# Kernel optimization log

Hardware: AMD Instinct MI355X
Metric: run time of the kernel (lower is better)

Reference implementation:

```python
import jax, jax.numpy as jnp
import numpy as np

EMBED_DIM = 128
D3 = EMBED_DIM // 3  # 42
K = 3  # k = min(3, N-1); N >> 4 so k is statically 3


def _local_density(points):
    # points: [B, N, 3] -> mean distance to 3 nearest neighbors, [B, N, 1]
    sq = jnp.sum(points * points, axis=-1)  # [B, N]
    d2 = sq[:, :, None] + sq[:, None, :] - 2.0 * jnp.einsum('bnd,bmd->bnm', points, points)
    dists = jnp.sqrt(jnp.maximum(d2, 1e-12))  # [B, N, N]
    N = points.shape[1]
    eye = jnp.eye(N, dtype=bool)
    dists = jnp.where(eye[None, :, :], jnp.inf, dists)
    # k smallest = -(k largest of negated)
    neg_topk, _ = jax.lax.top_k(-dists, K)  # [B, N, K]
    return jnp.mean(-neg_topk, axis=-1, keepdims=True)  # [B, N, 1]


def setup_inputs() -> dict:
    key = jax.random.key(0)
    ks = jax.random.split(key, 9)
    B, N = 8, 4096
    points = jax.random.normal(ks[0], (B, N, 3), dtype=jnp.float32)
    # PyTorch Linear init scale: U(-1/sqrt(fan_in), 1/sqrt(fan_in))
    def lin(k, fan_in, fan_out):
        k1, k2 = jax.random.split(k)
        bnd = 1.0 / np.sqrt(fan_in)
        W = jax.random.uniform(k1, (fan_in, fan_out), jnp.float32, -bnd, bnd)
        b = jax.random.uniform(k2, (fan_out,), jnp.float32, -bnd, bnd)
        return W, b
    W_rel, b_rel = lin(ks[1], 3, D3)
    W_dist, b_dist = lin(ks[2], 1, D3)
    W_dens, b_dens = lin(ks[3], 1, D3)
    W_out, b_out = lin(ks[4], 3 * D3, EMBED_DIM)
    return {"points": points, "W_rel": W_rel, "b_rel": b_rel,
            "W_dist": W_dist, "b_dist": b_dist, "W_dens": W_dens, "b_dens": b_dens,
            "W_out": W_out, "b_out": b_out}


def reference(points, W_rel, b_rel, W_dist, b_dist, W_dens, b_dens, W_out, b_out):
    centroid = jnp.mean(points, axis=1, keepdims=True)          # [B, 1, 3]
    relative_pos = points - centroid                             # [B, N, 3]
    rel_features = relative_pos @ W_rel + b_rel                  # [B, N, D3]
    centroid_dist = jnp.linalg.norm(relative_pos, axis=-1, keepdims=True)  # [B, N, 1]
    dist_features = centroid_dist @ W_dist + b_dist              # [B, N, D3]
    local_density = _local_density(points)                       # [B, N, 1]
    density_features = local_density @ W_dens + b_dens           # [B, N, D3]
    features = jnp.concatenate([rel_features, dist_features, density_features], axis=-1)
    return features @ W_out + b_out                              # [B, N, 128]
```

## Files before the change

kernel.cpp:

```cpp
#include <hip/hip_runtime.h>
#include <math.h>

#define NPTS 4096
#define NBATCH 8

#define WS_CENT 0
#define WS_COEF 32

__global__ void prep_kernel(const float* __restrict__ pts,
                            const float* __restrict__ W_rel, const float* __restrict__ b_rel,
                            const float* __restrict__ W_dist, const float* __restrict__ b_dist,
                            const float* __restrict__ W_dens, const float* __restrict__ b_dens,
                            const float* __restrict__ W_out, const float* __restrict__ b_out,
                            float* __restrict__ ws) {
    __shared__ float sx[256], sy[256], sz[256];
    if (blockIdx.x < NBATCH) {
        int b = blockIdx.x;
        const float* P = pts + (size_t)b * NPTS * 3;
        float ax = 0.f, ay = 0.f, az = 0.f;
        for (int n = threadIdx.x; n < NPTS; n += 256) {
            ax += P[3 * n + 0];
            ay += P[3 * n + 1];
            az += P[3 * n + 2];
        }
        sx[threadIdx.x] = ax; sy[threadIdx.x] = ay; sz[threadIdx.x] = az;
        __syncthreads();
        for (int off = 128; off > 0; off >>= 1) {
            if (threadIdx.x < off) {
                sx[threadIdx.x] += sx[threadIdx.x + off];
                sy[threadIdx.x] += sy[threadIdx.x + off];
                sz[threadIdx.x] += sz[threadIdx.x + off];
            }
            __syncthreads();
        }
        if (threadIdx.x == 0) {
            const float inv = 1.0f / (float)NPTS;
            ws[WS_CENT + 4 * b + 0] = sx[0] * inv;
            ws[WS_CENT + 4 * b + 1] = sy[0] * inv;
            ws[WS_CENT + 4 * b + 2] = sz[0] * inv;
        }
    } else if (threadIdx.x < 128) {
        int o = threadIdx.x;
        float a0 = 0.f, a1 = 0.f, a2 = 0.f, vd = 0.f, vl = 0.f, be = b_out[o];
        for (int j = 0; j < 42; ++j) {
            float w0 = W_out[j * 128 + o];
            float w1 = W_out[(42 + j) * 128 + o];
            float w2 = W_out[(84 + j) * 128 + o];
            a0 = fmaf(W_rel[j],      w0, a0);
            a1 = fmaf(W_rel[42 + j], w0, a1);
            a2 = fmaf(W_rel[84 + j], w0, a2);
            vd = fmaf(W_dist[j],     w1, vd);
            vl = fmaf(W_dens[j],     w2, vl);
            be = fmaf(b_rel[j], w0, be);
            be = fmaf(b_dist[j], w1, be);
            be = fmaf(b_dens[j], w2, be);
        }
        float* C = ws + WS_COEF;
        C[0 * 128 + o] = a0;
        C[1 * 128 + o] = a1;
        C[2 * 128 + o] = a2;
        C[3 * 128 + o] = vd;
        C[4 * 128 + o] = vl;
        C[5 * 128 + o] = be;
    }
}

#define INS3(t0, t1, t2, v)                                   \
    {                                                         \
        float n0 = fminf(t0, (v));                            \
        float n1 = __builtin_amdgcn_fmed3f(t0, t1, (v));      \
        float n2 = __builtin_amdgcn_fmed3f(t1, t2, (v));      \
        t0 = n0; t1 = n1; t2 = n2;                            \
    }

#define MERGE3(t0, t1, t2, m)                                 \
    {                                                         \
        float b0 = __shfl_xor(t0, m);                         \
        float b1 = __shfl_xor(t1, m);                         \
        float b2 = __shfl_xor(t2, m);                         \
        float X = fmaxf(t0, b0);                              \
        t0 = fminf(t0, b0);                                   \
        float Y = fminf(t1, b1);                              \
        float Z = fmaxf(X, Y);                                \
        t1 = fminf(X, Y);                                     \
        t2 = fminf(Z, fminf(t2, b2));                         \
    }

__launch_bounds__(1024, 8)
__global__ void density_out_kernel(const float* __restrict__ pts,
                                   const float* __restrict__ ws,
                                   float* __restrict__ out) {
    __shared__ float4 lp4[NPTS];
    __shared__ float dens[64];
    int b = blockIdx.x >> 6;
    int g = blockIdx.x & 63;
    int tid = threadIdx.x;

    {
        const float4* P4 = (const float4*)(pts + (size_t)b * NPTS * 3);
        float4 v0 = P4[3 * tid + 0];
        float4 v1 = P4[3 * tid + 1];
        float4 v2 = P4[3 * tid + 2];
        float x0 = v0.x, y0 = v0.y, z0 = v0.z;
        float x1 = v0.w, y1 = v1.x, z1 = v1.y;
        float x2 = v1.z, y2 = v1.w, z2 = v2.x;
        float x3 = v2.y, y3 = v2.z, z3 = v2.w;
        lp4[4 * tid + 0] = make_float4(x0, y0, z0, fmaf(x0, x0, fmaf(y0, y0, z0 * z0)));
        lp4[4 * tid + 1] = make_float4(x1, y1, z1, fmaf(x1, x1, fmaf(y1, y1, z1 * z1)));
        lp4[4 * tid + 2] = make_float4(x2, y2, z2, fmaf(x2, x2, fmaf(y2, y2, z2 * z2)));
        lp4[4 * tid + 3] = make_float4(x3, y3, z3, fmaf(x3, x3, fmaf(y3, y3, z3 * z3)));
    }
    __syncthreads();

    int w = tid >> 6;
    int lane = tid & 63;
    int lw = w << 2;
    int qb = (g << 6) + lw;

    float4 Q0 = lp4[qb + 0];
    float4 Q1 = lp4[qb + 1];
    float4 Q2 = lp4[qb + 2];
    float4 Q3 = lp4[qb + 3];
    float q0x = -2.f * Q0.x, q0y = -2.f * Q0.y, q0z = -2.f * Q0.z;
    float q1x = -2.f * Q1.x, q1y = -2.f * Q1.y, q1z = -2.f * Q1.z;
    float q2x = -2.f * Q2.x, q2y = -2.f * Q2.y, q2z = -2.f * Q2.z;
    float q3x = -2.f * Q3.x, q3y = -2.f * Q3.y, q3z = -2.f * Q3.z;

    float t00 = INFINITY, t01 = INFINITY, t02 = INFINITY;
    float t10 = INFINITY, t11 = INFINITY, t12 = INFINITY;
    float t20 = INFINITY, t21 = INFINITY, t22 = INFINITY;
    float t30 = INFINITY, t31 = INFINITY, t32 = INFINITY;

    #pragma unroll 4
    for (int tile = 0; tile < 64; ++tile) {
        float4 c = lp4[(tile << 6) + lane];
        float e0 = fmaf(q0x, c.x, fmaf(q0y, c.y, fmaf(q0z, c.z, c.w)));
        float e1 = fmaf(q1x, c.x, fmaf(q1y, c.y, fmaf(q1z, c.z, c.w)));
        float e2 = fmaf(q2x, c.x, fmaf(q2y, c.y, fmaf(q2z, c.z, c.w)));
        float e3 = fmaf(q3x, c.x, fmaf(q3y, c.y, fmaf(q3z, c.z, c.w)));
        INS3(t00, t01, t02, e0);
        INS3(t10, t11, t12, e1);
        INS3(t20, t21, t22, e2);
        INS3(t30, t31, t32, e3);
    }

    if (lane == lw + 0) { t00 = t01; t01 = t02; t02 = INFINITY; }
    if (lane == lw + 1) { t10 = t11; t11 = t12; t12 = INFINITY; }
    if (lane == lw + 2) { t20 = t21; t21 = t22; t22 = INFINITY; }
    if (lane == lw + 3) { t30 = t31; t31 = t32; t32 = INFINITY; }

    #pragma unroll
    for (int m = 1; m < 64; m <<= 1) {
        MERGE3(t00, t01, t02, m);
        MERGE3(t10, t11, t12, m);
        MERGE3(t20, t21, t22, m);
        MERGE3(t30, t31, t32, m);
    }

    if (lane == 0) {
        dens[lw + 0] = (sqrtf(fmaxf(t00 + Q0.w, 1e-12f)) + sqrtf(fmaxf(t01 + Q0.w, 1e-12f)) +
                        sqrtf(fmaxf(t02 + Q0.w, 1e-12f))) * (1.0f / 3.0f);
        dens[lw + 1] = (sqrtf(fmaxf(t10 + Q1.w, 1e-12f)) + sqrtf(fmaxf(t11 + Q1.w, 1e-12f)) +
                        sqrtf(fmaxf(t12 + Q1.w, 1e-12f))) * (1.0f / 3.0f);
        dens[lw + 2] = (sqrtf(fmaxf(t20 + Q2.w, 1e-12f)) + sqrtf(fmaxf(t21 + Q2.w, 1e-12f)) +
                        sqrtf(fmaxf(t22 + Q2.w, 1e-12f))) * (1.0f / 3.0f);
        dens[lw + 3] = (sqrtf(fmaxf(t30 + Q3.w, 1e-12f)) + sqrtf(fmaxf(t31 + Q3.w, 1e-12f)) +
                        sqrtf(fmaxf(t32 + Q3.w, 1e-12f))) * (1.0f / 3.0f);
    }
    __syncthreads();

    int r = tid >> 4;
    int c8 = (tid & 15) << 3;
    float4 p = lp4[(g << 6) + r];
    float cx = ws[WS_CENT + 4 * b + 0];
    float cy = ws[WS_CENT + 4 * b + 1];
    float cz = ws[WS_CENT + 4 * b + 2];
    float rx = p.x - cx, ry = p.y - cy, rz = p.z - cz;
    float cd = sqrtf(fmaf(rx, rx, fmaf(ry, ry, rz * rz)));
    float ld = dens[r];
    const float* C = ws + WS_COEF;
    float* orow = out + ((size_t)(b * NPTS + (g << 6) + r)) * 128;
    #pragma unroll
    for (int h = 0; h < 2; ++h) {
        int o = c8 + 4 * h;
        float4 A0 = *(const float4*)(C + 0 * 128 + o);
        float4 A1 = *(const float4*)(C + 1 * 128 + o);
        float4 A2 = *(const float4*)(C + 2 * 128 + o);
        float4 VD = *(const float4*)(C + 3 * 128 + o);
        float4 VL = *(const float4*)(C + 4 * 128 + o);
        float4 BE = *(const float4*)(C + 5 * 128 + o);
        float4 rv;
        rv.x = fmaf(rx, A0.x, fmaf(ry, A1.x, fmaf(rz, A2.x, fmaf(cd, VD.x, fmaf(ld, VL.x, BE.x)))));
        rv.y = fmaf(rx, A0.y, fmaf(ry, A1.y, fmaf(rz, A2.y, fmaf(cd, VD.y, fmaf(ld, VL.y, BE.y)))));
        rv.z = fmaf(rx, A0.z, fmaf(ry, A1.z, fmaf(rz, A2.z, fmaf(cd, VD.z, fmaf(ld, VL.z, BE.z)))));
        rv.w = fmaf(rx, A0.w, fmaf(ry, A1.w, fmaf(rz, A2.w, fmaf(cd, VD.w, fmaf(ld, VL.w, BE.w)))));
        *(float4*)(orow + o) = rv;
    }
}

extern "C" void kernel_launch(void* const* d_in, const int* in_sizes, int n_in,
                              void* d_out, int out_size, void* d_ws, size_t ws_size,
                              hipStream_t stream) {
    const float* pts    = (const float*)d_in[0];
    const float* W_rel  = (const float*)d_in[1];
    const float* b_rel  = (const float*)d_in[2];
    const float* W_dist = (const float*)d_in[3];
    const float* b_dist = (const float*)d_in[4];
    const float* W_dens = (const float*)d_in[5];
    const float* b_dens = (const float*)d_in[6];
    const float* W_out  = (const float*)d_in[7];
    const float* b_out  = (const float*)d_in[8];
    float* out = (float*)d_out;
    float* ws  = (float*)d_ws;

    hipLaunchKernelGGL(prep_kernel, dim3(NBATCH + 1), dim3(256), 0, stream,
                       pts, W_rel, b_rel, W_dist, b_dist, W_dens, b_dens, W_out, b_out, ws);
    hipLaunchKernelGGL(density_out_kernel, dim3(NBATCH * 64), dim3(1024), 0, stream,
                       pts, ws, out);
}
```

Baseline: 38.95 us.

## Fuse prep into density kernel, compute centroid and coefficients per block, 8 queries per wave

Removes the separate prep kernel: each block now computes the batch centroid with wave shuffles and redundantly folds the weight matrices into LDS coefficients. Each wave now handles 8 query points instead of 4, using readfirstlane to keep query coordinates scalar, which halves the grid to 256 blocks of 1024 threads. This saves a kernel launch and the global workspace round trip, and reuses each candidate LDS load across more queries. The costs are redundant weight folding in every block, fewer blocks to fill the device, and higher register pressure.

```diff
diff --git a/kernel.cpp b/kernel.cpp
--- a/kernel.cpp
+++ b/kernel.cpp
@@ -3,67 +3,6 @@
 
 #define NPTS 4096
 #define NBATCH 8
-
-#define WS_CENT 0
-#define WS_COEF 32
-
-__global__ void prep_kernel(const float* __restrict__ pts,
-                            const float* __restrict__ W_rel, const float* __restrict__ b_rel,
-                            const float* __restrict__ W_dist, const float* __restrict__ b_dist,
-                            const float* __restrict__ W_dens, const float* __restrict__ b_dens,
-                            const float* __restrict__ W_out, const float* __restrict__ b_out,
-                            float* __restrict__ ws) {
-    __shared__ float sx[256], sy[256], sz[256];
-    if (blockIdx.x < NBATCH) {
-        int b = blockIdx.x;
-        const float* P = pts + (size_t)b * NPTS * 3;
-        float ax = 0.f, ay = 0.f, az = 0.f;
-        for (int n = threadIdx.x; n < NPTS; n += 256) {
-            ax += P[3 * n + 0];
-            ay += P[3 * n + 1];
-            az += P[3 * n + 2];
-        }
-        sx[threadIdx.x] = ax; sy[threadIdx.x] = ay; sz[threadIdx.x] = az;
-        __syncthreads();
-        for (int off = 128; off > 0; off >>= 1) {
-            if (threadIdx.x < off) {
-                sx[threadIdx.x] += sx[threadIdx.x + off];
-                sy[threadIdx.x] += sy[threadIdx.x + off];
-                sz[threadIdx.x] += sz[threadIdx.x + off];
-            }
-            __syncthreads();
-        }
-        if (threadIdx.x == 0) {
-            const float inv = 1.0f / (float)NPTS;
-            ws[WS_CENT + 4 * b + 0] = sx[0] * inv;
-            ws[WS_CENT + 4 * b + 1] = sy[0] * inv;
-            ws[WS_CENT + 4 * b + 2] = sz[0] * inv;
-        }
-    } else if (threadIdx.x < 128) {
-        int o = threadIdx.x;
-        float a0 = 0.f, a1 = 0.f, a2 = 0.f, vd = 0.f, vl = 0.f, be = b_out[o];
-        for (int j = 0; j < 42; ++j) {
-            float w0 = W_out[j * 128 + o];
-            float w1 = W_out[(42 + j) * 128 + o];
-            float w2 = W_out[(84 + j) * 128 + o];
-            a0 = fmaf(W_rel[j],      w0, a0);
-            a1 = fmaf(W_rel[42 + j], w0, a1);
-            a2 = fmaf(W_rel[84 + j], w0, a2);
-            vd = fmaf(W_dist[j],     w1, vd);
-            vl = fmaf(W_dens[j],     w2, vl);
-            be = fmaf(b_rel[j], w0, be);
-            be = fmaf(b_dist[j], w1, be);
-            be = fmaf(b_dens[j], w2, be);
-        }
-        float* C = ws + WS_COEF;
-        C[0 * 128 + o] = a0;
-        C[1 * 128 + o] = a1;
-        C[2 * 128 + o] = a2;
-        C[3 * 128 + o] = vd;
-        C[4 * 128 + o] = vl;
-        C[5 * 128 + o] = be;
-    }
-}
 
 #define INS3(t0, t1, t2, v)                                   \
     {                                                         \
@@ -86,15 +25,51 @@
         t2 = fminf(Z, fminf(t2, b2));                         \
     }
 
-__launch_bounds__(1024, 8)
-__global__ void density_out_kernel(const float* __restrict__ pts,
-                                   const float* __restrict__ ws,
-                                   float* __restrict__ out) {
+#define RFL(x) __uint_as_float(__builtin_amdgcn_readfirstlane(__float_as_uint(x)))
+
+#define DECLQ(j)                                              \
+    float4 Q##j = lp4[qb + j];                                \
+    float qx##j = RFL(-2.0f * Q##j.x);                        \
+    float qy##j = RFL(-2.0f * Q##j.y);                        \
+    float qz##j = RFL(-2.0f * Q##j.z);                        \
+    float sq##j = RFL(Q##j.w);                                \
+    float t##j##0 = INFINITY, t##j##1 = INFINITY, t##j##2 = INFINITY;
+
+#define STEP(j)                                                             \
+    {                                                                       \
+        float e = fmaf(qx##j, c.x, fmaf(qy##j, c.y, fmaf(qz##j, c.z, c.w)));\
+        INS3(t##j##0, t##j##1, t##j##2, e);                                 \
+    }
+
+#define SELF(j)                                                             \
+    if (lane == (((w << 3) + j) & 63)) {                                    \
+        t##j##0 = t##j##1; t##j##1 = t##j##2; t##j##2 = INFINITY;           \
+    }
+
+#define MRG(j, m) MERGE3(t##j##0, t##j##1, t##j##2, m)
+
+#define DENS(j)                                                             \
+    float d##j = (sqrtf(fmaxf(t##j##0 + sq##j, 1e-12f)) +                   \
+                  sqrtf(fmaxf(t##j##1 + sq##j, 1e-12f)) +                   \
+                  sqrtf(fmaxf(t##j##2 + sq##j, 1e-12f))) * (1.0f / 3.0f);
+
+__launch_bounds__(1024, 4)
+__global__ void fused_kernel(const float* __restrict__ pts,
+                             const float* __restrict__ W_rel, const float* __restrict__ b_rel,
+                             const float* __restrict__ W_dist, const float* __restrict__ b_dist,
+                             const float* __restrict__ W_dens, const float* __restrict__ b_dens,
+                             const float* __restrict__ W_out, const float* __restrict__ b_out,
+                             float* __restrict__ out) {
     __shared__ float4 lp4[NPTS];
-    __shared__ float dens[64];
-    int b = blockIdx.x >> 6;
-    int g = blockIdx.x & 63;
+    __shared__ float4 cpart[16];
+    __shared__ float4 cent;
+    __shared__ __align__(16) float Clds[6][128];
+    __shared__ float dens[128];
+
+    int b = blockIdx.x >> 5;
+    int g = blockIdx.x & 31;
     int tid = threadIdx.x;
+    int w = tid >> 6, lane = tid & 63;
 
     {
         const float4* P4 = (const float4*)(pts + (size_t)b * NPTS * 3);
@@ -109,92 +84,102 @@
         lp4[4 * tid + 1] = make_float4(x1, y1, z1, fmaf(x1, x1, fmaf(y1, y1, z1 * z1)));
         lp4[4 * tid + 2] = make_float4(x2, y2, z2, fmaf(x2, x2, fmaf(y2, y2, z2 * z2)));
         lp4[4 * tid + 3] = make_float4(x3, y3, z3, fmaf(x3, x3, fmaf(y3, y3, z3 * z3)));
+        float sx = (x0 + x1) + (x2 + x3);
+        float sy = (y0 + y1) + (y2 + y3);
+        float sz = (z0 + z1) + (z2 + z3);
+        #pragma unroll
+        for (int m = 1; m < 64; m <<= 1) {
+            sx += __shfl_xor(sx, m);
+            sy += __shfl_xor(sy, m);
+            sz += __shfl_xor(sz, m);
+        }
+        if (lane == 0) cpart[w] = make_float4(sx, sy, sz, 0.f);
     }
     __syncthreads();
 
-    int w = tid >> 6;
-    int lane = tid & 63;
-    int lw = w << 2;
-    int qb = (g << 6) + lw;
-
-    float4 Q0 = lp4[qb + 0];
-    float4 Q1 = lp4[qb + 1];
-    float4 Q2 = lp4[qb + 2];
-    float4 Q3 = lp4[qb + 3];
-    float q0x = -2.f * Q0.x, q0y = -2.f * Q0.y, q0z = -2.f * Q0.z;
-    float q1x = -2.f * Q1.x, q1y = -2.f * Q1.y, q1z = -2.f * Q1.z;
-    float q2x = -2.f * Q2.x, q2y = -2.f * Q2.y, q2z = -2.f * Q2.z;
-    float q3x = -2.f * Q3.x, q3y = -2.f * Q3.y, q3z = -2.f * Q3.z;
-
-    float t00 = INFINITY, t01 = INFINITY, t02 = INFINITY;
-    float t10 = INFINITY, t11 = INFINITY, t12 = INFINITY;
-    float t20 = INFINITY, t21 = INFINITY, t22 = INFINITY;
-    float t30 = INFINITY, t31 = INFINITY, t32 = INFINITY;
+    if (w == 0 && lane < 16) {
+        float4 p = cpart[lane];
+        float cx = p.x, cy = p.y, cz = p.z;
+        #pragma unroll
+        for (int m = 1; m < 16; m <<= 1) {
+            cx += __shfl_xor(cx, m);
+            cy += __shfl_xor(cy, m);
+            cz += __shfl_xor(cz, m);
+        }
+        if (lane == 0) {
+            const float inv = 1.0f / (float)NPTS;
+            cent = make_float4(cx * inv, cy * inv, cz * inv, 0.f);
+        }
+    }
+    if (tid < 128) {
+        int o = tid;
+        float a0 = 0.f, a1 = 0.f, a2 = 0.f, vd = 0.f, vl = 0.f, be = b_out[o];
+        for (int j = 0; j < 42; ++j) {
+            float w0 = W_out[j * 128 + o];
+            float w1 = W_out[(42 + j) * 128 + o];
+            float w2 = W_out[(84 + j) * 128 + o];
+            a0 = fmaf(W_rel[j],      w0, a0);
+            a1 = fmaf(W_rel[42 + j], w0, a1);
+            a2 = fmaf(W_rel[84 + j], w0, a2);
+            vd = fmaf(W_dist[j],     w1, vd);
+            vl = fmaf(W_dens[j],     w2, vl);
+            be = fmaf(b_rel[j],  w0, be);
+            be = fmaf(b_dist[j], w1, be);
+            be = fmaf(b_dens[j], w2, be);
+        }
+        Clds[0][o] = a0; Clds[1][o] = a1; Clds[2][o] = a2;
+        Clds[3][o] = vd; Clds[4][o] = vl; Clds[5][o] = be;
+    }
+
+    int qb = (g << 7) + (w << 3);
+    DECLQ(0) DECLQ(1) DECLQ(2) DECLQ(3) DECLQ(4) DECLQ(5) DECLQ(6) DECLQ(7)
 
     #pragma unroll 4
     for (int tile = 0; tile < 64; ++tile) {
         float4 c = lp4[(tile << 6) + lane];
-        float e0 = fmaf(q0x, c.x, fmaf(q0y, c.y, fmaf(q0z, c.z, c.w)));
-        float e1 = fmaf(q1x, c.x, fmaf(q1y, c.y, fmaf(q1z, c.z, c.w)));
-        float e2 = fmaf(q2x, c.x, fmaf(q2y, c.y, fmaf(q2z, c.z, c.w)));
-        float e3 = fmaf(q3x, c.x, fmaf(q3y, c.y, fmaf(q3z, c.z, c.w)));
-        INS3(t00, t01, t02, e0);
-        INS3(t10, t11, t12, e1);
-        INS3(t20, t21, t22, e2);
-        INS3(t30, t31, t32, e3);
-    }
-
-    if (lane == lw + 0) { t00 = t01; t01 = t02; t02 = INFINITY; }
-    if (lane == lw + 1) { t10 = t11; t11 = t12; t12 = INFINITY; }
-    if (lane == lw + 2) { t20 = t21; t21 = t22; t22 = INFINITY; }
-    if (lane == lw + 3) { t30 = t31; t31 = t32; t32 = INFINITY; }
+        STEP(0) STEP(1) STEP(2) STEP(3) STEP(4) STEP(5) STEP(6) STEP(7)
+    }
+
+    SELF(0) SELF(1) SELF(2) SELF(3) SELF(4) SELF(5) SELF(6) SELF(7)
 
     #pragma unroll
     for (int m = 1; m < 64; m <<= 1) {
-        MERGE3(t00, t01, t02, m);
-        MERGE3(t10, t11, t12, m);
-        MERGE3(t20, t21, t22, m);
-        MERGE3(t30, t31, t32, m);
-    }
-
+        MRG(0, m) MRG(1, m) MRG(2, m) MRG(3, m)
+        MRG(4, m) MRG(5, m) MRG(6, m) MRG(7, m)
+    }
+
+    DENS(0) DENS(1) DENS(2) DENS(3) DENS(4) DENS(5) DENS(6) DENS(7)
     if (lane == 0) {
-        dens[lw + 0] = (sqrtf(fmaxf(t00 + Q0.w, 1e-12f)) + sqrtf(fmaxf(t01 + Q0.w, 1e-12f)) +
-                        sqrtf(fmaxf(t02 + Q0.w, 1e-12f))) * (1.0f / 3.0f);
-        dens[lw + 1] = (sqrtf(fmaxf(t10 + Q1.w, 1e-12f)) + sqrtf(fmaxf(t11 + Q1.w, 1e-12f)) +
-                        sqrtf(fmaxf(t12 + Q1.w, 1e-12f))) * (1.0f / 3.0f);
-        dens[lw + 2] = (sqrtf(fmaxf(t20 + Q2.w, 1e-12f)) + sqrtf(fmaxf(t21 + Q2.w, 1e-12f)) +
-                        sqrtf(fmaxf(t22 + Q2.w, 1e-12f))) * (1.0f / 3.0f);
-        dens[lw + 3] = (sqrtf(fmaxf(t30 + Q3.w, 1e-12f)) + sqrtf(fmaxf(t31 + Q3.w, 1e-12f)) +
-                        sqrtf(fmaxf(t32 + Q3.w, 1e-12f))) * (1.0f / 3.0f);
+        int db = w << 3;
+        dens[db + 0] = d0; dens[db + 1] = d1; dens[db + 2] = d2; dens[db + 3] = d3;
+        dens[db + 4] = d4; dens[db + 5] = d5; dens[db + 6] = d6; dens[db + 7] = d7;
     }
     __syncthreads();
 
-    int r = tid >> 4;
-    int c8 = (tid & 15) << 3;
-    float4 p = lp4[(g << 6) + r];
-    float cx = ws[WS_CENT + 4 * b + 0];
-    float cy = ws[WS_CENT + 4 * b + 1];
-    float cz = ws[WS_CENT + 4 * b + 2];
-    float rx = p.x - cx, ry = p.y - cy, rz = p.z - cz;
-    float cd = sqrtf(fmaf(rx, rx, fmaf(ry, ry, rz * rz)));
-    float ld = dens[r];
-    const float* C = ws + WS_COEF;
-    float* orow = out + ((size_t)(b * NPTS + (g << 6) + r)) * 128;
-    #pragma unroll
-    for (int h = 0; h < 2; ++h) {
-        int o = c8 + 4 * h;
-        float4 A0 = *(const float4*)(C + 0 * 128 + o);
-        float4 A1 = *(const float4*)(C + 1 * 128 + o);
-        float4 A2 = *(const float4*)(C + 2 * 128 + o);
-        float4 VD = *(const float4*)(C + 3 * 128 + o);
-        float4 VL = *(const float4*)(C + 4 * 128 + o);
-        float4 BE = *(const float4*)(C + 5 * 128 + o);
-        float4 rv;
-        rv.x = fmaf(rx, A0.x, fmaf(ry, A1.x, fmaf(rz, A2.x, fmaf(cd, VD.x, fmaf(ld, VL.x, BE.x)))));
-        rv.y = fmaf(rx, A0.y, fmaf(ry, A1.y, fmaf(rz, A2.y, fmaf(cd, VD.y, fmaf(ld, VL.y, BE.y)))));
-        rv.z = fmaf(rx, A0.z, fmaf(ry, A1.z, fmaf(rz, A2.z, fmaf(cd, VD.z, fmaf(ld, VL.z, BE.z)))));
-        rv.w = fmaf(rx, A0.w, fmaf(ry, A1.w, fmaf(rz, A2.w, fmaf(cd, VD.w, fmaf(ld, VL.w, BE.w)))));
-        *(float4*)(orow + o) = rv;
+    {
+        int r = tid >> 3;
+        int c16 = (tid & 7) << 4;
+        float4 p = lp4[(g << 7) + r];
+        float rx = p.x - cent.x, ry = p.y - cent.y, rz = p.z - cent.z;
+        float cd = sqrtf(fmaf(rx, rx, fmaf(ry, ry, rz * rz)));
+        float ld = dens[r];
+        float* orow = out + ((size_t)(b * NPTS + (g << 7) + r)) * 128;
+        #pragma unroll
+        for (int h = 0; h < 4; ++h) {
+            int o = c16 + 4 * h;
+            float4 A0 = *(const float4*)&Clds[0][o];
+            float4 A1 = *(const float4*)&Clds[1][o];
+            float4 A2 = *(const float4*)&Clds[2][o];
+            float4 VD = *(const float4*)&Clds[3][o];
+            float4 VL = *(const float4*)&Clds[4][o];
+            float4 BE = *(const float4*)&Clds[5][o];
+            float4 rv;
+            rv.x = fmaf(rx, A0.x, fmaf(ry, A1.x, fmaf(rz, A2.x, fmaf(cd, VD.x, fmaf(ld, VL.x, BE.x)))));
+            rv.y = fmaf(rx, A0.y, fmaf(ry, A1.y, fmaf(rz, A2.y, fmaf(cd, VD.y, fmaf(ld, VL.y, BE.y)))));
+            rv.z = fmaf(rx, A0.z, fmaf(ry, A1.z, fmaf(rz, A2.z, fmaf(cd, VD.z, fmaf(ld, VL.z, BE.z)))));
+            rv.w = fmaf(rx, A0.w, fmaf(ry, A1.w, fmaf(rz, A2.w, fmaf(cd, VD.w, fmaf(ld, VL.w, BE.w)))));
+            *(float4*)(orow + o) = rv;
+        }
     }
 }
 
@@ -211,10 +196,7 @@
     const float* W_out  = (const float*)d_in[7];
     const float* b_out  = (const float*)d_in[8];
     float* out = (float*)d_out;
-    float* ws  = (float*)d_ws;
-
-    hipLaunchKernelGGL(prep_kernel, dim3(NBATCH + 1), dim3(256), 0, stream,
-                       pts, W_rel, b_rel, W_dist, b_dist, W_dens, b_dens, W_out, b_out, ws);
-    hipLaunchKernelGGL(density_out_kernel, dim3(NBATCH * 64), dim3(1024), 0, stream,
-                       pts, ws, out);
+
+    hipLaunchKernelGGL(fused_kernel, dim3(NBATCH * 32), dim3(1024), 0, stream,
+                       pts, W_rel, b_rel, W_dist, b_dist, W_dens, b_dens, W_out, b_out, out);
 }
```

Result: slower. 39.94 us (+2.5%).
